# Performance work log

Hardware: AMD Instinct MI355X
Metric: run time of the kernel (lower is better)

## Reference

```python
import jax, jax.numpy as jnp
import numpy as np

B, IN_CH, H, W = 4, 1, 512, 512
DEPTH, WIDTH = 12, 2
DILATIONS = tuple(range(1, DEPTH + 1))


def setup_inputs() -> dict:
    key = jax.random.key(0)
    ks = jax.random.split(key, DEPTH + 2)
    inp = {"x": jax.random.normal(ks[0], (B, IN_CH, H, W), jnp.float32)}
    inp["bias"] = jax.random.normal(ks[1], (DEPTH * WIDTH,), jnp.float32) * 0.01
    for i in range(DEPTH):
        n_in = IN_CH + WIDTH * i
        # kaiming-ish scale for 3x3 kernel with n_in input channels
        inp[f"w{i}"] = jax.random.normal(ks[2 + i], (WIDTH, n_in, 3, 3), jnp.float32) / np.sqrt(9.0 * n_in)
    return inp


def _dilated_conv_relu(x, w, b, d):
    # msd_pytorch's conv2d_relu_forward: reflection-padded dilated 3x3 conv + bias + ReLU,
    # preserving spatial size (pad = dilation).
    xp = jnp.pad(x, ((0, 0), (0, 0), (d, d), (d, d)), mode='reflect')
    y = jax.lax.conv_general_dilated(
        xp, w, window_strides=(1, 1), padding='VALID',
        rhs_dilation=(d, d), dimension_numbers=('NCHW', 'OIHW', 'NCHW'))
    return jax.nn.relu(y + b[None, :, None, None])


def reference(x, bias, w0, w1, w2, w3, w4, w5, w6, w7, w8, w9, w10, w11):
    weights = (w0, w1, w2, w3, w4, w5, w6, w7, w8, w9, w10, w11)
    buf = x  # growing dense buffer: each layer consumes all previous channels
    for i, w in enumerate(weights):
        b = bias[i * WIDTH:(i + 1) * WIDTH]
        y = _dilated_conv_relu(buf, w, b, DILATIONS[i])
        buf = jnp.concatenate([buf, y], axis=1)
    return buf  # (B, IN_CH + DEPTH*WIDTH, H, W)
```

## Files before the change

### kernel.cpp

```cpp
#include <hip/hip_runtime.h>

#define HH 512
#define WW 512
#define NC 25
#define HWs (HH * WW)

__device__ __forceinline__ int refl(int p, int n) {
    p = (p < 0) ? -p : p;
    p = (p >= n) ? (2 * n - 2 - p) : p;
    return p;
}

__global__ __launch_bounds__(256) void copy_x_kernel(const float* __restrict__ x,
                                                     float* __restrict__ out) {
    int t = blockIdx.x * 256 + threadIdx.x;
    int b = t >> 16;
    int r = t & 65535;
    const float4* src = (const float4*)(x + (size_t)b * HWs);
    float4* dst = (float4*)(out + (size_t)b * NC * HWs);
    dst[r] = src[r];
}

template <int NIN, int DIL>
__global__ __launch_bounds__(256, 3) void msd_layer(const float* __restrict__ wts,
                                                    const float* __restrict__ bias,
                                                    float* __restrict__ buf,
                                                    int layer) {
    constexpr int M6 = 512 / (6 * DIL);
    constexpr int DM = DIL * M6;
    constexpr int SPAN = 6 * DM;
    constexpr int RT = 512 - SPAN;
    constexpr int TCH = (RT + 3) / 4;
    constexpr int IMT = 512 * DM;
    constexpr int NMAIN = 4 * IMT;

    int bid = blockIdx.x;
    {
        const int nblk = gridDim.x;
        const int q = nblk >> 3, r = nblk & 7;
        const int xcd = bid & 7, idx = bid >> 3;
        bid = (xcd < r ? xcd * (q + 1) : r * (q + 1) + (xcd - r) * q) + idx;
    }
    const int t = bid * 256 + threadIdx.x;

    const float b0 = bias[2 * layer];
    const float b1 = bias[2 * layer + 1];

    if (t < NMAIN) {
        const int img = t / IMT;
        const int u = t - img * IMT;
        const int bi = __builtin_amdgcn_readfirstlane(u >> 9);
        const int w = u & 511;
        const int k = bi / DIL, j = bi - k * DIL;
        const int h = 6 * DIL * k + j;

        int rowoff[8];
#pragma unroll
        for (int r = 0; r < 8; ++r) rowoff[r] = refl(h + (r - 1) * DIL, HH) * WW;
        int cw[3];
#pragma unroll
        for (int q = 0; q < 3; ++q) cw[q] = refl(w + (q - 1) * DIL, WW);

        float a0[6], a1[6];
#pragma unroll
        for (int al = 0; al < 6; ++al) { a0[al] = b0; a1[al] = b1; }
        const float* base = buf + (size_t)img * NC * HWs;

        const int c0 = bid - (bid / NIN) * NIN;

        float vA[8][3], vB[8][3];

        auto LD = [&](float (&v)[8][3], int c) {
            const float* plane = base + (size_t)c * HWs;
#pragma unroll
            for (int r = 0; r < 8; ++r) {
                const float* rowp = plane + rowoff[r];
#pragma unroll
                for (int q = 0; q < 3; ++q) v[r][q] = rowp[cw[q]];
            }
        };
        auto FM = [&](const float (&v)[8][3], int c) {
            float wk0[9], wk1[9];
#pragma unroll
            for (int kk = 0; kk < 9; ++kk) {
                wk0[kk] = wts[c * 9 + kk];
                wk1[kk] = wts[(NIN + c) * 9 + kk];
            }
#pragma unroll
            for (int al = 0; al < 6; ++al)
#pragma unroll
                for (int kr = 0; kr < 3; ++kr)
#pragma unroll
                    for (int kw = 0; kw < 3; ++kw) {
                        float vv = v[al + kr][kw];
                        a0[al] = fmaf(vv, wk0[kr * 3 + kw], a0[al]);
                        a1[al] = fmaf(vv, wk1[kr * 3 + kw], a1[al]);
                    }
        };

        LD(vA, c0);
#pragma unroll
        for (int i = 0; i < NIN; i += 2) {
            int cA = c0 + i;     cA -= (cA >= NIN) ? NIN : 0;
            int cB = c0 + i + 1; cB -= (cB >= NIN) ? NIN : 0;
            if (i + 1 < NIN) LD(vB, cB);
            FM(vA, cA);
            if (i + 1 >= NIN) break;
            int cN = c0 + i + 2; cN -= (cN >= NIN) ? NIN : 0;
            if (i + 2 < NIN) LD(vA, cN);
            FM(vB, cB);
        }

        float* o0 = buf + (size_t)(img * NC + NIN) * HWs;
        float* o1 = o0 + HWs;
#pragma unroll
        for (int al = 0; al < 6; ++al) {
            size_t off = (size_t)(h + al * DIL) * WW + (size_t)w;
            o0[off] = fmaxf(a0[al], 0.f);
            o1[off] = fmaxf(a1[al], 0.f);
        }
    } else if (RT > 0) {
        const int t2 = t - NMAIN;
        constexpr int PIT = 512 * TCH;
        const int img = t2 / PIT;
        const int u = t2 - img * PIT;
        const int s = __builtin_amdgcn_readfirstlane(u >> 9);
        const int w = u & 511;
        const int r0 = SPAN + 4 * s;

        int cw[3];
#pragma unroll
        for (int q = 0; q < 3; ++q) cw[q] = refl(w + (q - 1) * DIL, WW);
        int ro[3][4];
#pragma unroll
        for (int kr = 0; kr < 3; ++kr)
#pragma unroll
            for (int i = 0; i < 4; ++i)
                ro[kr][i] = refl(r0 + i + (kr - 1) * DIL, HH) * WW;

        float a0[4] = {b0, b0, b0, b0};
        float a1[4] = {b1, b1, b1, b1};
        const float* base = buf + (size_t)img * NC * HWs;

        for (int c = 0; c < NIN; ++c) {
            const float* plane = base + (size_t)c * HWs;
            float wk0[9], wk1[9];
#pragma unroll
            for (int kk = 0; kk < 9; ++kk) {
                wk0[kk] = wts[c * 9 + kk];
                wk1[kk] = wts[(NIN + c) * 9 + kk];
            }
#pragma unroll
            for (int i = 0; i < 4; ++i) {
                if (r0 + i < HH) {
#pragma unroll
                    for (int kr = 0; kr < 3; ++kr) {
                        const float* rowp = plane + ro[kr][i];
#pragma unroll
                        for (int kw = 0; kw < 3; ++kw) {
                            float vv = rowp[cw[kw]];
                            a0[i] = fmaf(vv, wk0[kr * 3 + kw], a0[i]);
                            a1[i] = fmaf(vv, wk1[kr * 3 + kw], a1[i]);
                        }
                    }
                }
            }
        }

        float* o0 = buf + (size_t)(img * NC + NIN) * HWs;
        float* o1 = o0 + HWs;
#pragma unroll
        for (int i = 0; i < 4; ++i) {
            if (r0 + i < HH) {
                size_t off = (size_t)(r0 + i) * WW + (size_t)w;
                o0[off] = fmaxf(a0[i], 0.f);
                o1[off] = fmaxf(a1[i], 0.f);
            }
        }
    }
}

extern "C" void kernel_launch(void* const* d_in, const int* in_sizes, int n_in,
                              void* d_out, int out_size, void* d_ws, size_t ws_size,
                              hipStream_t stream) {
    const float* x = (const float*)d_in[0];
    const float* bias = (const float*)d_in[1];
    float* out = (float*)d_out;

    copy_x_kernel<<<1024, 256, 0, stream>>>(x, out);

#define GBLK(dil) (8 * ((dil) * (512 / (6 * (dil)))) \
                 + 8 * (((512 - 6 * ((dil) * (512 / (6 * (dil))))) + 3) / 4))
#define LAYER(i, nin, dil) \
    msd_layer<nin, dil><<<GBLK(dil), 256, 0, stream>>>((const float*)d_in[2 + i], bias, out, i)

    LAYER(0, 1, 1);
    LAYER(1, 3, 2);
    LAYER(2, 5, 3);
    LAYER(3, 7, 4);
    LAYER(4, 9, 5);
    LAYER(5, 11, 6);
    LAYER(6, 13, 7);
    LAYER(7, 15, 8);
    LAYER(8, 17, 9);
    LAYER(9, 19, 10);
    LAYER(10, 21, 11);
    LAYER(11, 23, 12);
#undef LAYER
#undef GBLK
}
```

Baseline: 334.1 us.

## Add paired-column float2 kernel variant for even-dilation layers

Adds a second layer kernel for even dilations in which each thread computes two adjacent columns across 4 strided rows, using float2 loads and stores. Because the dilation is even, the horizontal taps stay float2-aligned, and scalar reflection fallbacks handle the image edges. The goal is fewer load instructions per output and wider memory transactions. In exchange, each thread uses more registers (the occupancy hint drops from 3 to 2), gets less vertical reuse (4 rows instead of 6), and the remainder path is larger. Odd dilations keep the original kernel.

```diff
diff --git a/kernel.cpp b/kernel.cpp
--- a/kernel.cpp
+++ b/kernel.cpp
@@ -22,10 +22,10 @@
 }
 
 template <int NIN, int DIL>
-__global__ __launch_bounds__(256, 3) void msd_layer(const float* __restrict__ wts,
-                                                    const float* __restrict__ bias,
-                                                    float* __restrict__ buf,
-                                                    int layer) {
+__global__ __launch_bounds__(256, 3) void msd_layer_s(const float* __restrict__ wts,
+                                                      const float* __restrict__ bias,
+                                                      float* __restrict__ buf,
+                                                      int layer) {
     constexpr int M6 = 512 / (6 * DIL);
     constexpr int DM = DIL * M6;
     constexpr int SPAN = 6 * DM;
@@ -180,6 +180,180 @@
     }
 }
 
+template <int NIN, int DIL>
+__global__ __launch_bounds__(256, 2) void msd_layer_p(const float* __restrict__ wts,
+                                                      const float* __restrict__ bias,
+                                                      float* __restrict__ buf,
+                                                      int layer) {
+    static_assert(DIL % 2 == 0, "pair kernel needs even dilation");
+    constexpr int M4 = 512 / (4 * DIL);
+    constexpr int DM = DIL * M4;
+    constexpr int SPAN = 4 * DM;
+    constexpr int RT = 512 - SPAN;
+    constexpr int TCH = (RT + 3) / 4;
+    constexpr int IMT = 256 * DM;
+    constexpr int NMAIN = 4 * IMT;
+    constexpr int HD = DIL / 2;
+
+    int bid = blockIdx.x;
+    {
+        const int nblk = gridDim.x;
+        const int q = nblk >> 3, r = nblk & 7;
+        const int xcd = bid & 7, idx = bid >> 3;
+        bid = (xcd < r ? xcd * (q + 1) : r * (q + 1) + (xcd - r) * q) + idx;
+    }
+    const int t = bid * 256 + threadIdx.x;
+
+    const float b0 = bias[2 * layer];
+    const float b1 = bias[2 * layer + 1];
+
+    if (t < NMAIN) {
+        const int img = t / IMT;
+        const int u = t - img * IMT;
+        const int bi = __builtin_amdgcn_readfirstlane(u >> 8);
+        const int lam = u & 255;
+        const int k = bi / DIL, j = bi - k * DIL;
+        const int h = 4 * DIL * k + j;
+
+        int rowoff[6];
+#pragma unroll
+        for (int r = 0; r < 6; ++r) rowoff[r] = refl(h + (r - 1) * DIL, HH) * WW;
+
+        const int pl = lam - HD, pc = lam, pr = lam + HD;
+        const bool eL = (pl < 0), eR = (pr > 255);
+        const int clx = refl(2 * lam - DIL, WW),     cly = refl(2 * lam + 1 - DIL, WW);
+        const int crx = refl(2 * lam + DIL, WW),     cry = refl(2 * lam + 1 + DIL, WW);
+
+        float a0x[4], a0y[4], a1x[4], a1y[4];
+#pragma unroll
+        for (int al = 0; al < 4; ++al) {
+            a0x[al] = b0; a0y[al] = b0; a1x[al] = b1; a1y[al] = b1;
+        }
+        const float* base = buf + (size_t)img * NC * HWs;
+
+        const int c0 = bid - (bid / NIN) * NIN;
+
+        float2 vA[6][3], vB[6][3];
+
+        auto LD = [&](float2 (&v)[6][3], int c) {
+            const float* plane = base + (size_t)c * HWs;
+#pragma unroll
+            for (int r = 0; r < 6; ++r) {
+                const float* rowp = plane + rowoff[r];
+                const float2* rp2 = (const float2*)rowp;
+                v[r][0] = eL ? make_float2(rowp[clx], rowp[cly]) : rp2[pl];
+                v[r][1] = rp2[pc];
+                v[r][2] = eR ? make_float2(rowp[crx], rowp[cry]) : rp2[pr];
+            }
+        };
+        auto FM = [&](const float2 (&v)[6][3], int c) {
+            float wk0[9], wk1[9];
+#pragma unroll
+            for (int kk = 0; kk < 9; ++kk) {
+                wk0[kk] = wts[c * 9 + kk];
+                wk1[kk] = wts[(NIN + c) * 9 + kk];
+            }
+#pragma unroll
+            for (int al = 0; al < 4; ++al)
+#pragma unroll
+                for (int kr = 0; kr < 3; ++kr)
+#pragma unroll
+                    for (int kw = 0; kw < 3; ++kw) {
+                        float2 vv = v[al + kr][kw];
+                        float w0 = wk0[kr * 3 + kw], w1 = wk1[kr * 3 + kw];
+                        a0x[al] = fmaf(vv.x, w0, a0x[al]);
+                        a0y[al] = fmaf(vv.y, w0, a0y[al]);
+                        a1x[al] = fmaf(vv.x, w1, a1x[al]);
+                        a1y[al] = fmaf(vv.y, w1, a1y[al]);
+                    }
+        };
+
+        {
+            int cA = c0;
+            LD(vA, cA);
+        }
+#pragma unroll
+        for (int i = 0; i < NIN; i += 2) {
+            int cA = c0 + i;     cA -= (cA >= NIN) ? NIN : 0;
+            int cB = c0 + i + 1; cB -= (cB >= NIN) ? NIN : 0;
+            if (i + 1 < NIN) LD(vB, cB);
+            FM(vA, cA);
+            if (i + 1 >= NIN) break;
+            int cN = c0 + i + 2; cN -= (cN >= NIN) ? NIN : 0;
+            if (i + 2 < NIN) LD(vA, cN);
+            FM(vB, cB);
+        }
+
+        float* o0 = buf + (size_t)(img * NC + NIN) * HWs;
+        float* o1 = o0 + HWs;
+#pragma unroll
+        for (int al = 0; al < 4; ++al) {
+            float2* p0 = (float2*)(o0 + (size_t)(h + al * DIL) * WW);
+            float2* p1 = (float2*)(o1 + (size_t)(h + al * DIL) * WW);
+            p0[lam] = make_float2(fmaxf(a0x[al], 0.f), fmaxf(a0y[al], 0.f));
+            p1[lam] = make_float2(fmaxf(a1x[al], 0.f), fmaxf(a1y[al], 0.f));
+        }
+    } else if (RT > 0) {
+        const int t2 = t - NMAIN;
+        constexpr int PIT = 512 * TCH;
+        const int img = t2 / PIT;
+        const int u = t2 - img * PIT;
+        const int s = __builtin_amdgcn_readfirstlane(u >> 9);
+        const int w = u & 511;
+        const int r0 = SPAN + 4 * s;
+
+        int cw[3];
+#pragma unroll
+        for (int q = 0; q < 3; ++q) cw[q] = refl(w + (q - 1) * DIL, WW);
+        int ro[3][4];
+#pragma unroll
+        for (int kr = 0; kr < 3; ++kr)
+#pragma unroll
+            for (int i = 0; i < 4; ++i)
+                ro[kr][i] = refl(r0 + i + (kr - 1) * DIL, HH) * WW;
+
+        float a0[4] = {b0, b0, b0, b0};
+        float a1[4] = {b1, b1, b1, b1};
+        const float* base = buf + (size_t)img * NC * HWs;
+
+        for (int c = 0; c < NIN; ++c) {
+            const float* plane = base + (size_t)c * HWs;
+            float wk0[9], wk1[9];
+#pragma unroll
+            for (int kk = 0; kk < 9; ++kk) {
+                wk0[kk] = wts[c * 9 + kk];
+                wk1[kk] = wts[(NIN + c) * 9 + kk];
+            }
+#pragma unroll
+            for (int i = 0; i < 4; ++i) {
+                if (r0 + i < HH) {
+#pragma unroll
+                    for (int kr = 0; kr < 3; ++kr) {
+                        const float* rowp = plane + ro[kr][i];
+#pragma unroll
+                        for (int kw = 0; kw < 3; ++kw) {
+                            float vv = rowp[cw[kw]];
+                            a0[i] = fmaf(vv, wk0[kr * 3 + kw], a0[i]);
+                            a1[i] = fmaf(vv, wk1[kr * 3 + kw], a1[i]);
+                        }
+                    }
+                }
+            }
+        }
+
+        float* o0 = buf + (size_t)(img * NC + NIN) * HWs;
+        float* o1 = o0 + HWs;
+#pragma unroll
+        for (int i = 0; i < 4; ++i) {
+            if (r0 + i < HH) {
+                size_t off = (size_t)(r0 + i) * WW + (size_t)w;
+                o0[off] = fmaxf(a0[i], 0.f);
+                o1[off] = fmaxf(a1[i], 0.f);
+            }
+        }
+    }
+}
+
 extern "C" void kernel_launch(void* const* d_in, const int* in_sizes, int n_in,
                               void* d_out, int out_size, void* d_ws, size_t ws_size,
                               hipStream_t stream) {
@@ -189,23 +363,29 @@
 
     copy_x_kernel<<<1024, 256, 0, stream>>>(x, out);
 
-#define GBLK(dil) (8 * ((dil) * (512 / (6 * (dil)))) \
-                 + 8 * (((512 - 6 * ((dil) * (512 / (6 * (dil))))) + 3) / 4))
-#define LAYER(i, nin, dil) \
-    msd_layer<nin, dil><<<GBLK(dil), 256, 0, stream>>>((const float*)d_in[2 + i], bias, out, i)
-
-    LAYER(0, 1, 1);
-    LAYER(1, 3, 2);
-    LAYER(2, 5, 3);
-    LAYER(3, 7, 4);
-    LAYER(4, 9, 5);
-    LAYER(5, 11, 6);
-    LAYER(6, 13, 7);
-    LAYER(7, 15, 8);
-    LAYER(8, 17, 9);
-    LAYER(9, 19, 10);
-    LAYER(10, 21, 11);
-    LAYER(11, 23, 12);
-#undef LAYER
-#undef GBLK
-}
+#define GBLKS(dil) (8 * ((dil) * (512 / (6 * (dil)))) \
+                  + 8 * (((512 - 6 * ((dil) * (512 / (6 * (dil))))) + 3) / 4))
+#define GBLKP(dil) (4 * ((dil) * (512 / (4 * (dil)))) \
+                  + 8 * (((512 - 4 * ((dil) * (512 / (4 * (dil))))) + 3) / 4))
+#define LAYERS(i, nin, dil) \
+    msd_layer_s<nin, dil><<<GBLKS(dil), 256, 0, stream>>>((const float*)d_in[2 + i], bias, out, i)
+#define LAYERP(i, nin, dil) \
+    msd_layer_p<nin, dil><<<GBLKP(dil), 256, 0, stream>>>((const float*)d_in[2 + i], bias, out, i)
+
+    LAYERS(0, 1, 1);
+    LAYERP(1, 3, 2);
+    LAYERS(2, 5, 3);
+    LAYERP(3, 7, 4);
+    LAYERS(4, 9, 5);
+    LAYERP(5, 11, 6);
+    LAYERS(6, 13, 7);
+    LAYERP(7, 15, 8);
+    LAYERS(8, 17, 9);
+    LAYERP(9, 19, 10);
+    LAYERS(10, 21, 11);
+    LAYERP(11, 23, 12);
+#undef LAYERS
+#undef LAYERP
+#undef GBLKS
+#undef GBLKP
+}
```

Measured after the change: 657.0 us. 96.7% more time.
